# Kernel tuning notes

Hardware: AMD Instinct MI355X
Metric: run time of the kernel (lower is better)

Reference implementation:

```python
import jax, jax.numpy as jnp
import numpy as np


def setup_inputs() -> dict:
    key = jax.random.key(0)
    k1, k2, k3 = jax.random.split(key, 3)
    B, T, C = 4, 2048, 1024
    x = jax.random.normal(k1, (B, T, C), dtype=jnp.float32)
    # Linear weights stored as (in, out) so y = x @ W + b
    w_attn = jax.random.normal(k2, (C, 3 * C), dtype=jnp.float32) * (1.0 / np.sqrt(C))
    b_attn = jnp.zeros((3 * C,), dtype=jnp.float32)
    w_proj = jax.random.normal(k3, (C, C), dtype=jnp.float32) * (1.0 / np.sqrt(C))
    b_proj = jnp.zeros((C,), dtype=jnp.float32)
    return {"x": x, "w_attn": w_attn, "b_attn": b_attn, "w_proj": w_proj, "b_proj": b_proj}


def reference(x, w_attn, b_attn, w_proj, b_proj):
    B, T, C = x.shape
    n_head = 16
    hd = C // n_head  # head dim = 64
    qkv = x @ w_attn + b_attn  # [B, T, 3C]
    q, k, v = jnp.split(qkv, 3, axis=-1)
    # [B, H, T, hd]
    q = q.reshape(B, T, n_head, hd).transpose(0, 2, 1, 3)
    k = k.reshape(B, T, n_head, hd).transpose(0, 2, 1, 3)
    v = v.reshape(B, T, n_head, hd).transpose(0, 2, 1, 3)
    scale = 1.0 / np.sqrt(hd).astype(np.float32)
    att = jnp.einsum("bhqd,bhkd->bhqk", q, k) * scale  # [B, H, T, T]
    causal = jnp.tril(jnp.ones((T, T), dtype=bool))
    att = jnp.where(causal[None, None], att, jnp.float32(-jnp.inf))
    att = jax.nn.softmax(att, axis=-1)
    y = jnp.einsum("bhqk,bhkd->bhqd", att, v)  # [B, H, T, hd]
    y = y.transpose(0, 2, 1, 3).reshape(B, T, C)
    return y @ w_proj + b_proj
```

## Files before the change

### kernel.cpp

```cpp
#include <hip/hip_runtime.h>

typedef __attribute__((ext_vector_type(8))) short short8;
typedef __attribute__((ext_vector_type(4))) float f32x4;
typedef __attribute__((ext_vector_type(16))) float f32x16;
typedef unsigned short u16;
typedef unsigned int u32;

__device__ __forceinline__ float bf2f(u16 u) {
    union { u32 i; float f; } x;
    x.i = ((u32)u) << 16;
    return x.f;
}

__device__ __forceinline__ u16 f2bf(float f) {
    union { float f; u32 i; } x;
    x.f = f;
    u32 r = x.i + 0x7fffu + ((x.i >> 16) & 1u);
    return (u16)(r >> 16);
}

__device__ __forceinline__ u32 cvt_pk_bf16(float lo, float hi) {
    u32 d;
    asm("v_cvt_pk_bf16_f32 %0, %1, %2" : "=v"(d) : "v"(lo), "v"(hi));
    return d;
}

__device__ __forceinline__ void gload_lds16(const u16* g, u16* l) {
    __builtin_amdgcn_global_load_lds(
        (const __attribute__((address_space(1))) void*)g,
        (__attribute__((address_space(3))) void*)l, 16, 0, 0);
}

__device__ __forceinline__ void pswap(u32& a, u32& b) {
#if __has_builtin(__builtin_amdgcn_permlane32_swap)
    auto r = __builtin_amdgcn_permlane32_swap(a, b, false, false);
    a = r[0];
    b = r[1];
#else
    const int l = (int)(threadIdx.x & 63);
    const u32 ax = __shfl(a, l ^ 32);
    const u32 bx = __shfl(b, l ^ 32);
    a = (l < 32) ? a : bx;
    b = (l < 32) ? ax : b;
#endif
}

#if __has_builtin(__builtin_amdgcn_exp2f)
#define EXP2F(x) __builtin_amdgcn_exp2f(x)
#else
#define EXP2F(x) exp2f(x)
#endif

#define K_SCALE 0.18033688f

__global__ __launch_bounds__(256) void convert_bf16(const float* __restrict__ in,
                                                    u16* __restrict__ out) {
    const long i = ((long)blockIdx.x * 256 + threadIdx.x) * 8;
    f32x4 v0 = *(const f32x4*)(in + i);
    f32x4 v1 = *(const f32x4*)(in + i + 4);
    short8 o;
#pragma unroll
    for (int j = 0; j < 4; ++j) o[j] = (short)f2bf(v0[j]);
#pragma unroll
    for (int j = 0; j < 4; ++j) o[4 + j] = (short)f2bf(v1[j]);
    *(short8*)(out + i) = o;
}

__global__ __launch_bounds__(256) void transpose_f32_bf16(const float* __restrict__ in,
                                                          u16* __restrict__ out,
                                                          int K, int N) {
    __shared__ float tile[32][33];
    const int nb = blockIdx.x * 32, kb = blockIdx.y * 32;
    const int tx = threadIdx.x, ty = threadIdx.y;
#pragma unroll
    for (int i = 0; i < 32; i += 8)
        tile[ty + i][tx] = in[(long)(kb + ty + i) * N + nb + tx];
    __syncthreads();
#pragma unroll
    for (int i = 0; i < 32; i += 8)
        out[(long)(nb + ty + i) * K + kb + tx] = f2bf(tile[tx][ty + i]);
}

__global__ __launch_bounds__(256) void transpose_v(const u16* __restrict__ qkv,
                                                   u16* __restrict__ vT) {
    __shared__ u16 tile[32][33];
    const int tb = blockIdx.x * 32;
    const int db = blockIdx.y * 32;
    const int bh = blockIdx.z;
    const int b = bh >> 4, h = bh & 15;
    const int tx = threadIdx.x, ty = threadIdx.y;
#pragma unroll
    for (int i = 0; i < 32; i += 8)
        tile[ty + i][tx] = qkv[((long)b * 2048 + tb + ty + i) * 3072 + 2048 + h * 64 + db + tx];
    __syncthreads();
#pragma unroll
    for (int i = 0; i < 32; i += 8)
        vT[((long)bh * 64 + db + ty + i) * 2048 + tb + tx] = tile[tx][ty + i];
}

__global__ __launch_bounds__(256, 2) void gemm_bf16_bt(
    const u16* __restrict__ A, int lda, const u16* __restrict__ BT,
    const float* __restrict__ bias, u16* __restrict__ C,
    int M, int N, int K) {
    __shared__ u16 As[128 * 32];
    __shared__ u16 Bs[128 * 32];
    const int tid = threadIdx.x;
    const int wv = tid >> 6, lane = tid & 63, quad = lane >> 4, L = lane & 15;
    const int wm = (wv >> 1) * 64, wn = (wv & 1) * 64;
    const long m0 = (long)blockIdx.y * 128;
    const long n0 = (long)blockIdx.x * 128;

    const u16* Ag = A + (m0 + wv * 32 + (lane >> 2)) * (long)lda + (lane & 3) * 8;
    const u16* Bg = BT + (n0 + wv * 32 + (lane >> 2)) * (long)K + (lane & 3) * 8;
    u16* AsW = &As[wv * 32 * 32];
    u16* BsW = &Bs[wv * 32 * 32];

    f32x4 zero4 = {0.f, 0.f, 0.f, 0.f};
    f32x4 acc[4][4];
#pragma unroll
    for (int i = 0; i < 4; ++i)
#pragma unroll
        for (int j = 0; j < 4; ++j) acc[i][j] = zero4;

    for (int kb = 0; kb < K; kb += 32) {
        __syncthreads();
        gload_lds16(Ag + kb, AsW);
        gload_lds16(Ag + kb + (long)16 * lda, AsW + 512);
        gload_lds16(Bg + kb, BsW);
        gload_lds16(Bg + kb + (long)16 * K, BsW + 512);
        __syncthreads();

        short8 af[4], bf[4];
#pragma unroll
        for (int mt = 0; mt < 4; ++mt)
            af[mt] = *(const short8*)&As[(wm + mt * 16 + L) * 32 + quad * 8];
#pragma unroll
        for (int nt = 0; nt < 4; ++nt)
            bf[nt] = *(const short8*)&Bs[(wn + nt * 16 + L) * 32 + quad * 8];
#pragma unroll
        for (int mt = 0; mt < 4; ++mt)
#pragma unroll
            for (int nt = 0; nt < 4; ++nt)
                acc[mt][nt] = __builtin_amdgcn_mfma_f32_16x16x32_bf16(
                    af[mt], bf[nt], acc[mt][nt], 0, 0, 0);
    }

#pragma unroll
    for (int nt = 0; nt < 4; ++nt) {
        const long col = n0 + wn + nt * 16 + L;
        const float bv = bias[col];
        const float scl = (col >= 1024 && col < 2048) ? K_SCALE : 1.0f;
#pragma unroll
        for (int mt = 0; mt < 4; ++mt)
#pragma unroll
            for (int r = 0; r < 4; ++r) {
                const long row = m0 + wm + mt * 16 + quad * 4 + r;
                C[row * N + col] = f2bf((acc[mt][nt][r] + bv) * scl);
            }
    }
}

__global__ __launch_bounds__(256, 2) void gemm_bf16_bn(
    const u16* __restrict__ A, int lda, const float* __restrict__ B,
    const float* __restrict__ bias, float* __restrict__ C,
    int M, int N, int K) {
    __shared__ u16 As[128 * 32];
    __shared__ u16 Bs[128 * 32];
    const int tid = threadIdx.x;
    const int wv = tid >> 6, lane = tid & 63, quad = lane >> 4, L = lane & 15;
    const int wm = (wv >> 1) * 64, wn = (wv & 1) * 64;
    const long m0 = (long)blockIdx.y * 128;
    const long n0 = (long)blockIdx.x * 128;

    const u16* Ag = A + (m0 + wv * 32 + (lane >> 2)) * (long)lda + (lane & 3) * 8;
    u16* AsW = &As[wv * 32 * 32];

    f32x4 zero4 = {0.f, 0.f, 0.f, 0.f};
    f32x4 acc[4][4];
#pragma unroll
    for (int i = 0; i < 4; ++i)
#pragma unroll
        for (int j = 0; j < 4; ++j) acc[i][j] = zero4;

    for (int kb = 0; kb < K; kb += 32) {
        short8 p[2];
#pragma unroll
        for (int i = 0; i < 2; ++i) {
            const int c = tid + i * 256;
            const int n = c >> 2, k8 = (c & 3) * 8;
            const float* bp = B + (long)(kb + k8) * N + n0 + n;
            float f[8];
#pragma unroll
            for (int j = 0; j < 8; ++j) f[j] = bp[(long)j * N];
            union { u32 d[4]; short8 v; } u;
#pragma unroll
            for (int j = 0; j < 4; ++j) u.d[j] = cvt_pk_bf16(f[2 * j], f[2 * j + 1]);
            p[i] = u.v;
        }
        __syncthreads();
        gload_lds16(Ag + kb, AsW);
        gload_lds16(Ag + kb + (long)16 * lda, AsW + 512);
        *(short8*)(&Bs[tid * 8]) = p[0];
        *(short8*)(&Bs[(tid + 256) * 8]) = p[1];
        __syncthreads();

        short8 af[4], bf[4];
#pragma unroll
        for (int mt = 0; mt < 4; ++mt)
            af[mt] = *(const short8*)&As[(wm + mt * 16 + L) * 32 + quad * 8];
#pragma unroll
        for (int nt = 0; nt < 4; ++nt)
            bf[nt] = *(const short8*)&Bs[(wn + nt * 16 + L) * 32 + quad * 8];
#pragma unroll
        for (int mt = 0; mt < 4; ++mt)
#pragma unroll
            for (int nt = 0; nt < 4; ++nt)
                acc[mt][nt] = __builtin_amdgcn_mfma_f32_16x16x32_bf16(
                    af[mt], bf[nt], acc[mt][nt], 0, 0, 0);
    }

#pragma unroll
    for (int nt = 0; nt < 4; ++nt) {
        const long col = n0 + wn + nt * 16 + L;
        const float bv = bias[col];
#pragma unroll
        for (int mt = 0; mt < 4; ++mt)
#pragma unroll
            for (int r = 0; r < 4; ++r) {
                const long row = m0 + wm + mt * 16 + quad * 4 + r;
                C[row * N + col] = acc[mt][nt][r] + bv;
            }
    }
}

#define AT_T 2048

__global__ __launch_bounds__(256) void attn_kernel(u16* __restrict__ qkv,
                                                   const u16* __restrict__ vT) {
    __shared__ u16 Kt[2][64 * 72];
    __shared__ u16 Vt[2][64 * 72];
    const int tid = threadIdx.x;
    const int wv = tid >> 6, lane = tid & 63;
    const int hi = lane >> 5, cc = lane & 31;
    const int bh = blockIdx.x;
    const int b = bh >> 4, h = bh & 15;
    const long rowbase = (long)b * AT_T;
    const long cbase = (long)h * 64;

    const int srow = tid >> 3, sc = tid & 7;
    const u16* Kg = qkv + (rowbase + srow) * 3072 + 1024 + cbase + sc * 8;
    const u16* Vg = vT + ((long)bh * 64 + srow) * 2048 + sc * 8;
    const int kLo = srow * 72 + sc * 8, kHi = (srow + 32) * 72 + sc * 8;

    short8 ones;
#pragma unroll
    for (int j = 0; j < 8; ++j) ones[j] = (cc == 0) ? (short)0x3F80 : (short)0;

    f32x16 z16;
#pragma unroll
    for (int r = 0; r < 16; ++r) z16[r] = 0.f;

    for (int pass = 0; pass < 2; ++pass) {
        const int qt = (pass == 0) ? (15 - (int)blockIdx.y) : (int)blockIdx.y;
        const int qw = qt * 128 + wv * 32;
        const int nkb = 2 * qt + 2;

        short8 qf[4];
#pragma unroll
        for (int ks = 0; ks < 4; ++ks)
            qf[ks] = *(const short8*)&qkv[(rowbase + qw + cc) * 3072 + cbase + ks * 16 + hi * 8];

        f32x16 accO0, accO1, accL;
#pragma unroll
        for (int r = 0; r < 16; ++r) { accO0[r] = 0.f; accO1[r] = 0.f; accL[r] = 0.f; }

        {
            *(short8*)&Kt[0][kLo] = *(const short8*)Kg;
            *(short8*)&Kt[0][kHi] = *(const short8*)(Kg + (long)32 * 3072);
            *(short8*)&Vt[0][kLo] = *(const short8*)Vg;
            *(short8*)&Vt[0][kHi] = *(const short8*)(Vg + (long)32 * 2048);
        }
        __syncthreads();

        int p = 0;
        for (int kb = 0; kb < nkb; ++kb) {
            const int k0 = kb * 64;
            const bool more = (kb + 1) < nkb;
            short8 kn0, kn1, vn0, vn1;
            if (more) {
                kn0 = *(const short8*)(Kg + (long)(k0 + 64) * 3072);
                kn1 = *(const short8*)(Kg + (long)(k0 + 96) * 3072);
                vn0 = *(const short8*)(Vg + k0 + 64);
                vn1 = *(const short8*)(Vg + (long)32 * 2048 + k0 + 64);
            }

#pragma unroll
            for (int hh = 0; hh < 2; ++hh) {
                const int kh = k0 + 32 * hh;
                if (kh <= qw) {
                    f32x16 s;
                    {
                        short8 kf = *(const short8*)&Kt[p][(32 * hh + cc) * 72 + hi * 8];
                        s = __builtin_amdgcn_mfma_f32_32x32x16_bf16(kf, qf[0], z16, 0, 0, 0);
                    }
#pragma unroll
                    for (int ks = 1; ks < 4; ++ks) {
                        short8 kf = *(const short8*)&Kt[p][(32 * hh + cc) * 72 + ks * 16 + hi * 8];
                        s = __builtin_amdgcn_mfma_f32_32x32x16_bf16(kf, qf[ks], s, 0, 0, 0);
                    }
                    float pe[16];
                    if (kh == qw) {
#pragma unroll
                        for (int r = 0; r < 16; ++r) {
                            const int key = (r & 3) + 8 * (r >> 2) + 4 * hi;
                            const float e = EXP2F(s[r]);
                            pe[r] = (key <= cc) ? e : 0.f;
                        }
                    } else {
#pragma unroll
                        for (int r = 0; r < 16; ++r) pe[r] = EXP2F(s[r]);
                    }

                    short8 pa[2];
#pragma unroll
                    for (int ks = 0; ks < 2; ++ks) {
                        u32 wA = cvt_pk_bf16(pe[8 * ks + 0], pe[8 * ks + 1]);
                        u32 wB = cvt_pk_bf16(pe[8 * ks + 2], pe[8 * ks + 3]);
                        u32 wC = cvt_pk_bf16(pe[8 * ks + 4], pe[8 * ks + 5]);
                        u32 wD = cvt_pk_bf16(pe[8 * ks + 6], pe[8 * ks + 7]);
                        pswap(wA, wC);
                        pswap(wB, wD);
                        union { u32 d[4]; short8 v; } u;
                        u.d[0] = wA; u.d[1] = wB; u.d[2] = wC; u.d[3] = wD;
                        pa[ks] = u.v;
                    }

                    accL = __builtin_amdgcn_mfma_f32_32x32x16_bf16(pa[0], ones, accL, 0, 0, 0);
                    accL = __builtin_amdgcn_mfma_f32_32x32x16_bf16(pa[1], ones, accL, 0, 0, 0);
#pragma unroll
                    for (int ks = 0; ks < 2; ++ks) {
                        short8 vf0 = *(const short8*)&Vt[p][cc * 72 + 32 * hh + ks * 16 + hi * 8];
                        short8 vf1 = *(const short8*)&Vt[p][(32 + cc) * 72 + 32 * hh + ks * 16 + hi * 8];
                        accO0 = __builtin_amdgcn_mfma_f32_32x32x16_bf16(pa[ks], vf0, accO0, 0, 0, 0);
                        accO1 = __builtin_amdgcn_mfma_f32_32x32x16_bf16(pa[ks], vf1, accO1, 0, 0, 0);
                    }
                }
            }

            if (more) {
                *(short8*)&Kt[p ^ 1][kLo] = kn0;
                *(short8*)&Kt[p ^ 1][kHi] = kn1;
                *(short8*)&Vt[p ^ 1][kLo] = vn0;
                *(short8*)&Vt[p ^ 1][kHi] = vn1;
            }
            __syncthreads();
            p ^= 1;
        }

#pragma unroll
        for (int r = 0; r < 16; ++r) {
            const float l = __shfl(accL[r], lane & 32);
            const float inv = 1.f / l;
            const int q = (r & 3) + 8 * (r >> 2) + 4 * hi;
            const long orow = (rowbase + qw + q) * 3072 + cbase;
            qkv[orow + cc] = f2bf(accO0[r] * inv);
            qkv[orow + 32 + cc] = f2bf(accO1[r] * inv);
        }
    }
}

extern "C" void kernel_launch(void* const* d_in, const int* in_sizes, int n_in,
                              void* d_out, int out_size, void* d_ws, size_t ws_size,
                              hipStream_t stream) {
    const float* x      = (const float*)d_in[0];
    const float* w_attn = (const float*)d_in[1];
    const float* b_attn = (const float*)d_in[2];
    const float* w_proj = (const float*)d_in[3];
    const float* b_proj = (const float*)d_in[4];
    float* out = (float*)d_out;

    u16* qkv = (u16*)d_ws;
    u16* xb  = (u16*)d_out;
    u16* wTa = (u16*)((char*)d_out + 16777216);
    u16* vT  = (u16*)d_out;

    convert_bf16<<<4096, 256, 0, stream>>>(x, xb);
    transpose_f32_bf16<<<dim3(3072 / 32, 1024 / 32), dim3(32, 8), 0, stream>>>(
        w_attn, wTa, 1024, 3072);
    gemm_bf16_bt<<<dim3(3072 / 128, 8192 / 128), 256, 0, stream>>>(
        xb, 1024, wTa, b_attn, qkv, 8192, 3072, 1024);
    transpose_v<<<dim3(64, 2, 64), dim3(32, 8), 0, stream>>>(qkv, vT);
    attn_kernel<<<dim3(64, 8), 256, 0, stream>>>(qkv, vT);
    gemm_bf16_bn<<<dim3(1024 / 128, 8192 / 128), 256, 0, stream>>>(
        qkv, 3072, w_proj, b_proj, out, 8192, 1024, 1024);
}
```

Measured before the change: 277.3 us.

## Triple-buffer QKV GEMM LDS loads and merge prep conversion kernels

```diff
diff --git a/kernel.cpp b/kernel.cpp
--- a/kernel.cpp
+++ b/kernel.cpp
@@ -53,32 +53,34 @@
 
 #define K_SCALE 0.18033688f
 
-__global__ __launch_bounds__(256) void convert_bf16(const float* __restrict__ in,
-                                                    u16* __restrict__ out) {
-    const long i = ((long)blockIdx.x * 256 + threadIdx.x) * 8;
-    f32x4 v0 = *(const f32x4*)(in + i);
-    f32x4 v1 = *(const f32x4*)(in + i + 4);
-    short8 o;
-#pragma unroll
-    for (int j = 0; j < 4; ++j) o[j] = (short)f2bf(v0[j]);
-#pragma unroll
-    for (int j = 0; j < 4; ++j) o[4 + j] = (short)f2bf(v1[j]);
-    *(short8*)(out + i) = o;
-}
-
-__global__ __launch_bounds__(256) void transpose_f32_bf16(const float* __restrict__ in,
-                                                          u16* __restrict__ out,
-                                                          int K, int N) {
+__global__ __launch_bounds__(256) void prep_kernel(const float* __restrict__ x,
+                                                   u16* __restrict__ xb,
+                                                   const float* __restrict__ w_attn,
+                                                   u16* __restrict__ wTa) {
     __shared__ float tile[32][33];
-    const int nb = blockIdx.x * 32, kb = blockIdx.y * 32;
-    const int tx = threadIdx.x, ty = threadIdx.y;
-#pragma unroll
-    for (int i = 0; i < 32; i += 8)
-        tile[ty + i][tx] = in[(long)(kb + ty + i) * N + nb + tx];
-    __syncthreads();
-#pragma unroll
-    for (int i = 0; i < 32; i += 8)
-        out[(long)(nb + ty + i) * K + kb + tx] = f2bf(tile[tx][ty + i]);
+    const int tid = threadIdx.x;
+    if (blockIdx.x < 4096) {
+        const long i = ((long)blockIdx.x * 256 + tid) * 8;
+        f32x4 v0 = *(const f32x4*)(x + i);
+        f32x4 v1 = *(const f32x4*)(x + i + 4);
+        short8 o;
+#pragma unroll
+        for (int j = 0; j < 4; ++j) o[j] = (short)f2bf(v0[j]);
+#pragma unroll
+        for (int j = 0; j < 4; ++j) o[4 + j] = (short)f2bf(v1[j]);
+        *(short8*)(xb + i) = o;
+    } else {
+        const int bid = blockIdx.x - 4096;
+        const int nb = (bid % 96) * 32, kb = (bid / 96) * 32;
+        const int tx = tid & 31, ty = tid >> 5;
+#pragma unroll
+        for (int i = 0; i < 32; i += 8)
+            tile[ty + i][tx] = w_attn[(long)(kb + ty + i) * 3072 + nb + tx];
+        __syncthreads();
+#pragma unroll
+        for (int i = 0; i < 32; i += 8)
+            wTa[(long)(nb + ty + i) * 1024 + kb + tx] = f2bf(tile[tx][ty + i]);
+    }
 }
 
 __global__ __launch_bounds__(256) void transpose_v(const u16* __restrict__ qkv,
@@ -98,12 +100,35 @@
         vT[((long)bh * 64 + db + ty + i) * 2048 + tb + tx] = tile[tx][ty + i];
 }
 
-__global__ __launch_bounds__(256, 2) void gemm_bf16_bt(
+#define G1_STAGE(KOFF, SLOT)                                                  \
+    gload_lds16(Ag + (KOFF), &As[(SLOT)*4096 + wbase]);                       \
+    gload_lds16(Ag + (KOFF) + (long)16 * lda, &As[(SLOT)*4096 + wbase + 512]);\
+    gload_lds16(Bg + (KOFF), &Bs[(SLOT)*4096 + wbase]);                       \
+    gload_lds16(Bg + (KOFF) + (long)16 * K, &Bs[(SLOT)*4096 + wbase + 512]);
+
+#define G1_COMPUTE(SLOT)                                                      \
+    {                                                                         \
+        short8 af[4], bf[4];                                                  \
+        _Pragma("unroll")                                                     \
+        for (int mt = 0; mt < 4; ++mt)                                        \
+            af[mt] = *(const short8*)&As[(SLOT)*4096 + (wm + mt*16 + L)*32 + quad*8]; \
+        _Pragma("unroll")                                                     \
+        for (int nt = 0; nt < 4; ++nt)                                        \
+            bf[nt] = *(const short8*)&Bs[(SLOT)*4096 + (wn + nt*16 + L)*32 + quad*8]; \
+        _Pragma("unroll")                                                     \
+        for (int mt = 0; mt < 4; ++mt)                                        \
+            _Pragma("unroll")                                                 \
+            for (int nt = 0; nt < 4; ++nt)                                    \
+                acc[mt][nt] = __builtin_amdgcn_mfma_f32_16x16x32_bf16(        \
+                    af[mt], bf[nt], acc[mt][nt], 0, 0, 0);                    \
+    }
+
+__global__ __launch_bounds__(256, 3) void gemm_bf16_bt(
     const u16* __restrict__ A, int lda, const u16* __restrict__ BT,
     const float* __restrict__ bias, u16* __restrict__ C,
     int M, int N, int K) {
-    __shared__ u16 As[128 * 32];
-    __shared__ u16 Bs[128 * 32];
+    __shared__ __align__(16) u16 As[3 * 128 * 32];
+    __shared__ __align__(16) u16 Bs[3 * 128 * 32];
     const int tid = threadIdx.x;
     const int wv = tid >> 6, lane = tid & 63, quad = lane >> 4, L = lane & 15;
     const int wm = (wv >> 1) * 64, wn = (wv & 1) * 64;
@@ -112,8 +137,7 @@
 
     const u16* Ag = A + (m0 + wv * 32 + (lane >> 2)) * (long)lda + (lane & 3) * 8;
     const u16* Bg = BT + (n0 + wv * 32 + (lane >> 2)) * (long)K + (lane & 3) * 8;
-    u16* AsW = &As[wv * 32 * 32];
-    u16* BsW = &Bs[wv * 32 * 32];
+    const int wbase = wv * 1024;
 
     f32x4 zero4 = {0.f, 0.f, 0.f, 0.f};
     f32x4 acc[4][4];
@@ -122,28 +146,25 @@
 #pragma unroll
         for (int j = 0; j < 4; ++j) acc[i][j] = zero4;
 
-    for (int kb = 0; kb < K; kb += 32) {
-        __syncthreads();
-        gload_lds16(Ag + kb, AsW);
-        gload_lds16(Ag + kb + (long)16 * lda, AsW + 512);
-        gload_lds16(Bg + kb, BsW);
-        gload_lds16(Bg + kb + (long)16 * K, BsW + 512);
-        __syncthreads();
-
-        short8 af[4], bf[4];
-#pragma unroll
-        for (int mt = 0; mt < 4; ++mt)
-            af[mt] = *(const short8*)&As[(wm + mt * 16 + L) * 32 + quad * 8];
-#pragma unroll
-        for (int nt = 0; nt < 4; ++nt)
-            bf[nt] = *(const short8*)&Bs[(wn + nt * 16 + L) * 32 + quad * 8];
-#pragma unroll
-        for (int mt = 0; mt < 4; ++mt)
-#pragma unroll
-            for (int nt = 0; nt < 4; ++nt)
-                acc[mt][nt] = __builtin_amdgcn_mfma_f32_16x16x32_bf16(
-                    af[mt], bf[nt], acc[mt][nt], 0, 0, 0);
-    }
+    G1_STAGE(0, 0);
+    G1_STAGE(32, 1);
+
+    int slot = 0, s2 = 2;
+    for (int kb = 0; kb + 64 < K; kb += 32) {
+        asm volatile("s_waitcnt vmcnt(4)" ::: "memory");
+        __builtin_amdgcn_s_barrier();
+        G1_STAGE(kb + 64, s2);
+        G1_COMPUTE(slot);
+        slot = (slot + 1 == 3) ? 0 : slot + 1;
+        s2 = (s2 + 1 == 3) ? 0 : s2 + 1;
+    }
+    asm volatile("s_waitcnt vmcnt(4)" ::: "memory");
+    __builtin_amdgcn_s_barrier();
+    G1_COMPUTE(slot);
+    slot = (slot + 1 == 3) ? 0 : slot + 1;
+    asm volatile("s_waitcnt vmcnt(0)" ::: "memory");
+    __builtin_amdgcn_s_barrier();
+    G1_COMPUTE(slot);
 
 #pragma unroll
     for (int nt = 0; nt < 4; ++nt) {
@@ -164,8 +185,8 @@
     const u16* __restrict__ A, int lda, const float* __restrict__ B,
     const float* __restrict__ bias, float* __restrict__ C,
     int M, int N, int K) {
-    __shared__ u16 As[128 * 32];
-    __shared__ u16 Bs[128 * 32];
+    __shared__ __align__(16) u16 As[128 * 32];
+    __shared__ __align__(16) u16 Bs[128 * 32];
     const int tid = threadIdx.x;
     const int wv = tid >> 6, lane = tid & 63, quad = lane >> 4, L = lane & 15;
     const int wm = (wv >> 1) * 64, wn = (wv & 1) * 64;
@@ -384,9 +405,7 @@
     u16* wTa = (u16*)((char*)d_out + 16777216);
     u16* vT  = (u16*)d_out;
 
-    convert_bf16<<<4096, 256, 0, stream>>>(x, xb);
-    transpose_f32_bf16<<<dim3(3072 / 32, 1024 / 32), dim3(32, 8), 0, stream>>>(
-        w_attn, wTa, 1024, 3072);
+    prep_kernel<<<4096 + 3072, 256, 0, stream>>>(x, xb, w_attn, wTa);
     gemm_bf16_bt<<<dim3(3072 / 128, 8192 / 128), 256, 0, stream>>>(
         xb, 1024, wTa, b_attn, qkv, 8192, 3072, 1024);
     transpose_v<<<dim3(64, 2, 64), dim3(32, 8), 0, stream>>>(qkv, vT);
```

New measurement: 281.3 us. No clear change (+1.4%).
